# Optimization experiments

Measured on AMD Instinct MI355X. Metric: run time of the kernel, lower is better.

## Reference

```python
import jax, jax.numpy as jnp
import numpy as np

WIN = (8, 8)          # window height/width -> seq_len n = 64
GAMMA = 16            # channel groups (s)
BLOCKS = 1024         # num_blocks == number of windows w
GATE_DIM = 256        # dim // chunks
EPS = 1e-5


def _rel_indices(win):
    # Quadratic relative-position features [n, n, 3] = (dx, dy, dx^2+dy^2)
    w, h = win
    ind = np.arange(h)[None, :] - np.arange(w)[:, None]            # (w, h)
    indx = np.tile(ind, (h, w))                                    # (n, n)
    indy = np.repeat(np.repeat(ind, h, axis=0), w, axis=1).T       # (n, n)
    indd = indx ** 2 + indy ** 2
    return jnp.asarray(np.stack([indx, indy, indd], axis=-1), dtype=jnp.float32)


def setup_inputs() -> dict:
    key = jax.random.key(0)
    k0, k1, k2 = jax.random.split(key, 3)
    b = 4
    n = WIN[0] * WIN[1]
    return {
        "x": jax.random.normal(k0, (b, BLOCKS, n, 2 * GATE_DIM), dtype=jnp.float32),
        "norm_weight": jnp.ones((GATE_DIM,), jnp.float32),
        "norm_bias": jnp.zeros((GATE_DIM,), jnp.float32),
        "attention_centers": 0.01 * jax.random.normal(k1, (BLOCKS * GAMMA, 2), jnp.float32),
        "attention_spreads": 1.0 + 0.01 * jax.random.normal(k2, (BLOCKS * GAMMA,), jnp.float32),
        "token_proj_n_bias": jnp.zeros((BLOCKS, n, 1), jnp.float32),
    }


def reference(x, norm_weight, norm_bias, attention_centers, attention_spreads, token_proj_n_bias):
    b, w, n, d = x.shape
    # chunk into gate halves: u mixed spatially, v is the gate
    u, v = jnp.split(x, 2, axis=-1)                                # [b,w,n,gd] each
    # LayerNorm over channel dim (biased variance, as torch)
    mean = u.mean(-1, keepdims=True)
    var = u.var(-1, keepdims=True)
    u = (u - mean) * jax.lax.rsqrt(var + EPS) * norm_weight + norm_bias
    # quadratic positional weights (QuaMap.forward_qua_pos)
    mu1, mu2 = attention_centers[:, 0], attention_centers[:, 1]
    a = attention_spreads ** 2
    pos_proj = jnp.stack([a * mu1, a * mu2, -0.5 * jnp.ones_like(mu1)], axis=-1)  # [g*w, 3]
    rel = _rel_indices(WIN)                                        # [n,n,3]
    pos_score = jnp.einsum('mnd,bd->bmn', rel, pos_proj)           # [g*w, n, n]
    win_weight = jax.nn.softmax(pos_score, axis=-1)
    # rearrange '(s b) m n -> b m n s' with s=gamma
    win_weight = win_weight.reshape(GAMMA, w, n, n).transpose(1, 2, 3, 0)  # [w,m,n,s]
    # rearrange 'b w n (v s) -> b w n v s'
    vdim = u.shape[-1] // GAMMA
    uu = u.reshape(b, w, n, vdim, GAMMA)
    # windowed spatial mixing + per-window bias
    mixed = jnp.einsum('wmns,bwnvs->bwmvs', win_weight, uu)
    mixed = mixed + token_proj_n_bias[None, :, :, None, :]          # [1,w,n,1,1]
    u = mixed.reshape(b, w, n, vdim * GAMMA)
    return u * v
```

## Files before the change

kernel.cpp:

```cpp
#include <hip/hip_runtime.h>
#include <cstdint>

#if __has_builtin(__builtin_amdgcn_exp2f)
#define EXP2F(x) __builtin_amdgcn_exp2f(x)
#else
#define EXP2F(x) exp2f(x)
#endif

typedef _Float16 half8 __attribute__((ext_vector_type(8)));
typedef float    f32x4 __attribute__((ext_vector_type(4)));


__global__ __launch_bounds__(512, 6) void sgating_kernel(
    const float* __restrict__ x,
    const float* __restrict__ norm_w,
    const float* __restrict__ norm_b,
    const float* __restrict__ centers,
    const float* __restrict__ spreads,
    const float* __restrict__ tbias,
    float* __restrict__ out)
{
    __shared__ __align__(16) float smem[12288];
    _Float16* Us = (_Float16*)smem;
    float*    Qm = smem + 8192;

    const int t     = threadIdx.x;
    const int wv    = t >> 6;
    const int lane  = t & 63;
    const int bw    = blockIdx.x;
    const int w_idx = bw & 1023;
    const size_t xbase = (size_t)bw * (64 * 512);
    const size_t obase = (size_t)bw * (64 * 256);

    {
        const float4 w4 = *(const float4*)(norm_w + lane * 4);
        const float4 b4 = *(const float4*)(norm_b + lane * 4);
        half8 uar[4];
#pragma unroll
        for (int r = 0; r < 8; ++r) {
            const int n = wv * 8 + r;
            const float4 u = *(const float4*)(x + xbase + (size_t)n * 512 + lane * 4);
            float s  = u.x + u.y + u.z + u.w;
            float sq = u.x*u.x + u.y*u.y + u.z*u.z + u.w*u.w;
#pragma unroll
            for (int off = 1; off < 64; off <<= 1) {
                s  += __shfl_xor(s, off);
                sq += __shfl_xor(sq, off);
            }
            const float mean = s * (1.0f/256.0f);
            const float var  = sq * (1.0f/256.0f) - mean*mean;
            const float rstd = rsqrtf(var + 1e-5f);
            uar[0][r] = (_Float16)((u.x - mean)*rstd*w4.x + b4.x);
            uar[1][r] = (_Float16)((u.y - mean)*rstd*w4.y + b4.y);
            uar[2][r] = (_Float16)((u.z - mean)*rstd*w4.z + b4.z);
            uar[3][r] = (_Float16)((u.w - mean)*rstd*w4.w + b4.w);
        }
#pragma unroll
        for (int j = 0; j < 4; ++j) {
            const int d  = lane * 4 + j;
            const int s  = d & 15;
            const int vd = d >> 4;
            const int nb = wv ^ (vd & 7);
            *(half8*)(Us + (s << 10) + (vd << 6) + (nb << 3)) = uar[j];
        }
    }
    __syncthreads();

    const int m16 = lane & 15;
    const int g   = lane >> 4;
    const float LOG2E = 1.4426950408889634f;
    const float C2    = 0.72134752044448f;
    const float mx  = (float)(m16 & 7);
    const float myb = (float)(m16 >> 3);

    const int sA = wv, sB = wv + 8;

    float bias4[4];
#pragma unroll
    for (int nt = 0; nt < 4; ++nt)
        bias4[nt] = tbias[w_idx * 64 + nt * 16 + m16];

    float aylA, aylB, sxA, sxB;
    half8 exhA, exhB;
    {
        const int hbA = (sA << 10) | w_idx;
        const int hbB = (sB << 10) | w_idx;
        float aq = spreads[hbA]; aq *= aq;
        const float axlA = aq * centers[2*hbA] * LOG2E;
        aylA = aq * centers[2*hbA + 1] * LOG2E;
        aq = spreads[hbB]; aq *= aq;
        const float axlB = aq * centers[2*hbB] * LOG2E;
        aylB = aq * centers[2*hbB + 1] * LOG2E;
        sxA = 0.f; sxB = 0.f;
#pragma unroll
        for (int j = 0; j < 8; ++j) {
            const float dx = (float)j - mx;
            const float eA = EXP2F(dx * fmaf(-C2, dx, axlA));
            const float eB = EXP2F(dx * fmaf(-C2, dx, axlB));
            sxA += eA; sxB += eB;
            exhA[j] = (_Float16)eA;
            exhB[j] = (_Float16)eB;
        }
    }

    auto compute_quarter = [&](int nt, f32x4& vOutA, f32x4& vOutB) {
        const float my = (float)(2*nt) + myb;
        f32x4 aA = (f32x4){0.f,0.f,0.f,0.f};
        f32x4 aB = (f32x4){0.f,0.f,0.f,0.f};
        float rsA = 0.f, rsB = 0.f;
#pragma unroll
        for (int kt = 0; kt < 2; ++kt) {
            const int nb = (g + 4*kt) ^ (m16 & 7);
            const half8 uA = *(const half8*)(Us + (sA << 10) + (m16 << 6) + (nb << 3));
            const half8 uB = *(const half8*)(Us + (sB << 10) + (m16 << 6) + (nb << 3));
            const float dy  = my - (float)(g + 4*kt);
            const float eA = EXP2F(dy * fmaf(-C2, dy, aylA));
            const float eB = EXP2F(dy * fmaf(-C2, dy, aylB));
            rsA += eA; rsB += eB;
            const _Float16 ehA = (_Float16)eA;
            const _Float16 ehB = (_Float16)eB;
            half8 wA, wB;
#pragma unroll
            for (int j = 0; j < 8; ++j) {
                wA[j] = exhA[j] * ehA;
                wB[j] = exhB[j] * ehB;
            }
            aA = __builtin_amdgcn_mfma_f32_16x16x32_f16(uA, wA, aA, 0, 0, 0);
            aB = __builtin_amdgcn_mfma_f32_16x16x32_f16(uB, wB, aB, 0, 0, 0);
        }
        float rA = rsA * sxA;
        rA += __shfl_xor(rA, 16); rA += __shfl_xor(rA, 32);
        float rB = rsB * sxB;
        rB += __shfl_xor(rB, 16); rB += __shfl_xor(rB, 32);
        const float iA = 1.0f / rA;
        const float iB = 1.0f / rB;
        const float bm = bias4[nt];
#pragma unroll
        for (int j = 0; j < 4; ++j) {
            vOutA[j] = aA[j] * iA + bm;
            vOutB[j] = aB[j] * iB + bm;
        }
    };

    f32x4 vA, vB, nA, nB;
    compute_quarter(0, vA, vB);

#pragma unroll
    for (int nt = 0; nt < 4; ++nt) {
        const int swz = (m16 & 7) << 2;
        *(f32x4*)(Qm + (m16 << 8) + ((sA * 16 + g * 4) ^ swz)) = vA;
        *(f32x4*)(Qm + (m16 << 8) + ((sB * 16 + g * 4) ^ swz)) = vB;
        __syncthreads();

        if (nt < 3) compute_quarter(nt + 1, nA, nB);

#pragma unroll
        for (int k = 0; k < 2; ++k) {
            const int mr = wv + 8 * k;
            const int m  = nt * 16 + mr;
            const int c4 = lane * 4;
            const int vd = c4 >> 4;
            const int s0 = c4 & 15;
            const int sw2 = (m & 7) << 2;
            float4 mxv;
            mxv.x = Qm[(mr << 8) + ((((s0 + 0) << 4) + vd) ^ sw2)];
            mxv.y = Qm[(mr << 8) + ((((s0 + 1) << 4) + vd) ^ sw2)];
            mxv.z = Qm[(mr << 8) + ((((s0 + 2) << 4) + vd) ^ sw2)];
            mxv.w = Qm[(mr << 8) + ((((s0 + 3) << 4) + vd) ^ sw2)];
            const float4 vv = *(const float4*)(x + xbase + (size_t)m * 512 + 256 + c4);
            float4 o;
            o.x = mxv.x * vv.x; o.y = mxv.y * vv.y;
            o.z = mxv.z * vv.z; o.w = mxv.w * vv.w;
            *(float4*)(out + obase + m * 256 + c4) = o;
        }

        if (nt < 3) {
            __syncthreads();
            vA = nA; vB = nB;
        }
    }
}

extern "C" void kernel_launch(void* const* d_in, const int* in_sizes, int n_in,
                              void* d_out, int out_size, void* d_ws, size_t ws_size,
                              hipStream_t stream) {
    const float* x       = (const float*)d_in[0];
    const float* norm_w  = (const float*)d_in[1];
    const float* norm_b  = (const float*)d_in[2];
    const float* centers = (const float*)d_in[3];
    const float* spreads = (const float*)d_in[4];
    const float* tbias   = (const float*)d_in[5];
    float* out = (float*)d_out;

    const int nbw = in_sizes[0] / (64 * 512);
    hipLaunchKernelGGL(sgating_kernel, dim3(nbw), dim3(512), 0, stream,
                       x, norm_w, norm_b, centers, spreads, tbias, out);
}
```

Before: 157.5 us.

## Prefetch gate half into fp16 registers and precompute separable softmax exponent tables

The gate half v is now loaded in the LayerNorm prologue, alongside u, and kept in registers as fp16. Token rows are reassigned to waves (n = r*8+wv) so each wave later consumes exactly the rows it prefetched, which removes the global reads from the epilogue. The separable softmax exponentials are precomputed into a 16-entry table per lane with the x/y roles swapped, and output uses nontemporal stores. Launch bounds drop to 4 waves/SIMD. This trades register pressure and fp16 rounding of the gate values for more memory-level parallelism and fewer exp calls.

```diff
diff --git a/kernel.cpp b/kernel.cpp
--- a/kernel.cpp
+++ b/kernel.cpp
@@ -8,10 +8,11 @@
 #endif
 
 typedef _Float16 half8 __attribute__((ext_vector_type(8)));
+typedef _Float16 half4 __attribute__((ext_vector_type(4)));
 typedef float    f32x4 __attribute__((ext_vector_type(4)));
 
 
-__global__ __launch_bounds__(512, 6) void sgating_kernel(
+__global__ __launch_bounds__(512, 4) void sgating_kernel(
     const float* __restrict__ x,
     const float* __restrict__ norm_w,
     const float* __restrict__ norm_b,
@@ -32,14 +33,20 @@
     const size_t xbase = (size_t)bw * (64 * 512);
     const size_t obase = (size_t)bw * (64 * 256);
 
+    half4 vreg[8];
+
     {
         const float4 w4 = *(const float4*)(norm_w + lane * 4);
         const float4 b4 = *(const float4*)(norm_b + lane * 4);
         half8 uar[4];
 #pragma unroll
         for (int r = 0; r < 8; ++r) {
-            const int n = wv * 8 + r;
-            const float4 u = *(const float4*)(x + xbase + (size_t)n * 512 + lane * 4);
+            const int n = r * 8 + wv;
+            const float* rowp = x + xbase + (size_t)n * 512 + lane * 4;
+            const float4 u  = *(const float4*)(rowp);
+            const float4 vv = *(const float4*)(rowp + 256);
+            vreg[r][0] = (_Float16)vv.x; vreg[r][1] = (_Float16)vv.y;
+            vreg[r][2] = (_Float16)vv.z; vreg[r][3] = (_Float16)vv.w;
             float s  = u.x + u.y + u.z + u.w;
             float sq = u.x*u.x + u.y*u.y + u.z*u.z + u.w*u.w;
 #pragma unroll
@@ -60,8 +67,8 @@
             const int d  = lane * 4 + j;
             const int s  = d & 15;
             const int vd = d >> 4;
-            const int nb = wv ^ (vd & 7);
-            *(half8*)(Us + (s << 10) + (vd << 6) + (nb << 3)) = uar[j];
+            const int qb = wv ^ (vd & 7);
+            *(half8*)(Us + (s << 10) + (vd << 6) + (qb << 3)) = uar[j];
         }
     }
     __syncthreads();
@@ -72,7 +79,6 @@
     const float C2    = 0.72134752044448f;
     const float mx  = (float)(m16 & 7);
     const float myb = (float)(m16 >> 3);
-
     const int sA = wv, sB = wv + 8;
 
     float bias4[4];
@@ -80,105 +86,127 @@
     for (int nt = 0; nt < 4; ++nt)
         bias4[nt] = tbias[w_idx * 64 + nt * 16 + m16];
 
-    float aylA, aylB, sxA, sxB;
-    half8 exhA, exhB;
+    float    exfA[2], exfB[2];
+    _Float16 exhA[2], exhB[2];
+    half8 EYA_[2], EYB_[2];
     {
         const int hbA = (sA << 10) | w_idx;
         const int hbB = (sB << 10) | w_idx;
         float aq = spreads[hbA]; aq *= aq;
-        const float axlA = aq * centers[2*hbA] * LOG2E;
-        aylA = aq * centers[2*hbA + 1] * LOG2E;
+        const float axlA = aq * centers[2*hbA]     * LOG2E;
+        const float aylA = aq * centers[2*hbA + 1] * LOG2E;
         aq = spreads[hbB]; aq *= aq;
-        const float axlB = aq * centers[2*hbB] * LOG2E;
-        aylB = aq * centers[2*hbB + 1] * LOG2E;
-        sxA = 0.f; sxB = 0.f;
-#pragma unroll
-        for (int j = 0; j < 8; ++j) {
-            const float dx = (float)j - mx;
+        const float axlB = aq * centers[2*hbB]     * LOG2E;
+        const float aylB = aq * centers[2*hbB + 1] * LOG2E;
+#pragma unroll
+        for (int kt = 0; kt < 2; ++kt) {
+            const float dx = (float)(g + 4*kt) - mx;
             const float eA = EXP2F(dx * fmaf(-C2, dx, axlA));
             const float eB = EXP2F(dx * fmaf(-C2, dx, axlB));
-            sxA += eA; sxB += eB;
-            exhA[j] = (_Float16)eA;
-            exhB[j] = (_Float16)eB;
+            exfA[kt] = eA; exhA[kt] = (_Float16)eA;
+            exfB[kt] = eB; exhB[kt] = (_Float16)eB;
+        }
+#pragma unroll
+        for (int i = 0; i < 16; ++i) {
+            const float dy = (float)(i - 7) + myb;
+            const _Float16 eA = (i < 14) ? (_Float16)EXP2F(dy * fmaf(-C2, dy, aylA)) : (_Float16)0.f;
+            const _Float16 eB = (i < 14) ? (_Float16)EXP2F(dy * fmaf(-C2, dy, aylB)) : (_Float16)0.f;
+            if (i < 8) { EYA_[0][i] = eA; EYB_[0][i] = eB; }
+            else       { EYA_[1][i-8] = eA; EYB_[1][i-8] = eB; }
         }
     }
 
-    auto compute_quarter = [&](int nt, f32x4& vOutA, f32x4& vOutB) {
-        const float my = (float)(2*nt) + myb;
-        f32x4 aA = (f32x4){0.f,0.f,0.f,0.f};
-        f32x4 aB = (f32x4){0.f,0.f,0.f,0.f};
-        float rsA = 0.f, rsB = 0.f;
-#pragma unroll
-        for (int kt = 0; kt < 2; ++kt) {
-            const int nb = (g + 4*kt) ^ (m16 & 7);
-            const half8 uA = *(const half8*)(Us + (sA << 10) + (m16 << 6) + (nb << 3));
-            const half8 uB = *(const half8*)(Us + (sB << 10) + (m16 << 6) + (nb << 3));
-            const float dy  = my - (float)(g + 4*kt);
-            const float eA = EXP2F(dy * fmaf(-C2, dy, aylA));
-            const float eB = EXP2F(dy * fmaf(-C2, dy, aylB));
-            rsA += eA; rsB += eB;
-            const _Float16 ehA = (_Float16)eA;
-            const _Float16 ehB = (_Float16)eB;
-            half8 wA, wB;
-#pragma unroll
-            for (int j = 0; j < 8; ++j) {
-                wA[j] = exhA[j] * ehA;
-                wB[j] = exhB[j] * ehB;
-            }
-            aA = __builtin_amdgcn_mfma_f32_16x16x32_f16(uA, wA, aA, 0, 0, 0);
-            aB = __builtin_amdgcn_mfma_f32_16x16x32_f16(uB, wB, aB, 0, 0, 0);
-        }
-        float rA = rsA * sxA;
-        rA += __shfl_xor(rA, 16); rA += __shfl_xor(rA, 32);
-        float rB = rsB * sxB;
-        rB += __shfl_xor(rB, 16); rB += __shfl_xor(rB, 32);
-        const float iA = 1.0f / rA;
-        const float iB = 1.0f / rB;
-        const float bm = bias4[nt];
-#pragma unroll
-        for (int j = 0; j < 4; ++j) {
-            vOutA[j] = aA[j] * iA + bm;
-            vOutB[j] = aB[j] * iB + bm;
-        }
-    };
-
-    f32x4 vA, vB, nA, nB;
-    compute_quarter(0, vA, vB);
-
-#pragma unroll
-    for (int nt = 0; nt < 4; ++nt) {
-        const int swz = (m16 & 7) << 2;
-        *(f32x4*)(Qm + (m16 << 8) + ((sA * 16 + g * 4) ^ swz)) = vA;
-        *(f32x4*)(Qm + (m16 << 8) + ((sB * 16 + g * 4) ^ swz)) = vB;
-        __syncthreads();
-
-        if (nt < 3) compute_quarter(nt + 1, nA, nB);
-
-#pragma unroll
-        for (int k = 0; k < 2; ++k) {
-            const int mr = wv + 8 * k;
-            const int m  = nt * 16 + mr;
-            const int c4 = lane * 4;
-            const int vd = c4 >> 4;
-            const int s0 = c4 & 15;
-            const int sw2 = (m & 7) << 2;
-            float4 mxv;
-            mxv.x = Qm[(mr << 8) + ((((s0 + 0) << 4) + vd) ^ sw2)];
-            mxv.y = Qm[(mr << 8) + ((((s0 + 1) << 4) + vd) ^ sw2)];
-            mxv.z = Qm[(mr << 8) + ((((s0 + 2) << 4) + vd) ^ sw2)];
-            mxv.w = Qm[(mr << 8) + ((((s0 + 3) << 4) + vd) ^ sw2)];
-            const float4 vv = *(const float4*)(x + xbase + (size_t)m * 512 + 256 + c4);
-            float4 o;
-            o.x = mxv.x * vv.x; o.y = mxv.y * vv.y;
-            o.z = mxv.z * vv.z; o.w = mxv.w * vv.w;
-            *(float4*)(out + obase + m * 256 + c4) = o;
-        }
-
-        if (nt < 3) {
-            __syncthreads();
-            vA = nA; vB = nB;
-        }
-    }
+#define EYAT(I) ((I) < 8 ? EYA_[0][(I)] : EYA_[1][(I)-8])
+#define EYBT(I) ((I) < 8 ? EYB_[0][(I)] : EYB_[1][(I)-8])
+
+#define CQ(NT, vOutA, vOutB) do {                                              \
+    f32x4 aA = (f32x4){0.f,0.f,0.f,0.f};                                       \
+    f32x4 aB = (f32x4){0.f,0.f,0.f,0.f};                                       \
+    half8 eyA8, eyB8;                                                          \
+    float syA = 0.f, syB = 0.f;                                                \
+    _Pragma("unroll") for (int j = 0; j < 8; ++j) {                            \
+        const _Float16 ea = EYAT(2*(NT)+7-j);                                  \
+        const _Float16 eb = EYBT(2*(NT)+7-j);                                  \
+        eyA8[j] = ea; eyB8[j] = eb;                                            \
+        syA += (float)ea; syB += (float)eb;                                    \
+    }                                                                          \
+    _Pragma("unroll") for (int kt = 0; kt < 2; ++kt) {                         \
+        const int qb = (g + 4*kt) ^ (m16 & 7);                                 \
+        const half8 uA = *(const half8*)(Us + (sA<<10) + (m16<<6) + (qb<<3));  \
+        const half8 uB = *(const half8*)(Us + (sB<<10) + (m16<<6) + (qb<<3));  \
+        half8 wA, wB;                                                          \
+        _Pragma("unroll") for (int j = 0; j < 8; ++j) {                        \
+            wA[j] = eyA8[j] * exhA[kt];                                        \
+            wB[j] = eyB8[j] * exhB[kt];                                        \
+        }                                                                      \
+        aA = __builtin_amdgcn_mfma_f32_16x16x32_f16(uA, wA, aA, 0, 0, 0);      \
+        aB = __builtin_amdgcn_mfma_f32_16x16x32_f16(uB, wB, aB, 0, 0, 0);      \
+    }                                                                          \
+    float rA = (exfA[0] + exfA[1]) * syA;                                      \
+    rA += __shfl_xor(rA, 16); rA += __shfl_xor(rA, 32);                        \
+    float rB = (exfB[0] + exfB[1]) * syB;                                      \
+    rB += __shfl_xor(rB, 16); rB += __shfl_xor(rB, 32);                        \
+    const float iA = 1.0f / rA;                                                \
+    const float iB = 1.0f / rB;                                                \
+    const float bm = bias4[(NT)];                                              \
+    _Pragma("unroll") for (int j = 0; j < 4; ++j) {                            \
+        vOutA[j] = aA[j]*iA + bm;                                              \
+        vOutB[j] = aB[j]*iB + bm;                                              \
+    }                                                                          \
+} while (0)
+
+#define WRITEQ(vA_, vB_) do {                                                  \
+    const int swz = (m16 & 7) << 2;                                            \
+    *(f32x4*)(Qm + (m16<<8) + ((sA*16 + g*4) ^ swz)) = vA_;                    \
+    *(f32x4*)(Qm + (m16<<8) + ((sB*16 + g*4) ^ swz)) = vB_;                    \
+} while (0)
+
+#define EPIK(NT, K) do {                                                       \
+    const int mr  = wv + 8*(K);                                                \
+    const int m   = (NT)*16 + mr;                                              \
+    const int c4  = lane * 4;                                                  \
+    const int vd  = c4 >> 4;                                                   \
+    const int s0  = c4 & 15;                                                   \
+    const int sw2 = (m & 7) << 2;                                              \
+    f32x4 mxv;                                                                 \
+    mxv[0] = Qm[(mr<<8) + ((((s0+0)<<4)+vd) ^ sw2)];                           \
+    mxv[1] = Qm[(mr<<8) + ((((s0+1)<<4)+vd) ^ sw2)];                           \
+    mxv[2] = Qm[(mr<<8) + ((((s0+2)<<4)+vd) ^ sw2)];                           \
+    mxv[3] = Qm[(mr<<8) + ((((s0+3)<<4)+vd) ^ sw2)];                           \
+    const half4 vh = vreg[2*(NT)+(K)];                                         \
+    f32x4 o;                                                                   \
+    o[0] = mxv[0] * (float)vh[0]; o[1] = mxv[1] * (float)vh[1];                \
+    o[2] = mxv[2] * (float)vh[2]; o[3] = mxv[3] * (float)vh[3];                \
+    __builtin_nontemporal_store(o, (f32x4*)(out + obase + m*256 + c4));        \
+} while (0)
+
+    f32x4 cA, cB, nA2, nB2;
+    CQ(0, cA, cB);
+
+    WRITEQ(cA, cB);
+    __syncthreads();
+    CQ(1, nA2, nB2);
+    EPIK(0, 0); EPIK(0, 1);
+    __syncthreads();
+    cA = nA2; cB = nB2;
+
+    WRITEQ(cA, cB);
+    __syncthreads();
+    CQ(2, nA2, nB2);
+    EPIK(1, 0); EPIK(1, 1);
+    __syncthreads();
+    cA = nA2; cB = nB2;
+
+    WRITEQ(cA, cB);
+    __syncthreads();
+    CQ(3, nA2, nB2);
+    EPIK(2, 0); EPIK(2, 1);
+    __syncthreads();
+    cA = nA2; cB = nB2;
+
+    WRITEQ(cA, cB);
+    __syncthreads();
+    EPIK(3, 0); EPIK(3, 1);
 }
 
 extern "C" void kernel_launch(void* const* d_in, const int* in_sizes, int n_in,
```

After: 156.3 us. No clear change (-0.8%).
